# Performance work log

Measured on AMD Instinct MI355X. Metric: run time of the kernel, lower is better.

Reference implementation:

```python
import jax, jax.numpy as jnp
import numpy as np

B, N, K, D, H = 16, 4096, 64, 1024, 8
ITERS = 2
DH = D // H


def _ln(x, g, b, eps=1e-5):
    m = x.mean(-1, keepdims=True)
    v = ((x - m) ** 2).mean(-1, keepdims=True)
    return (x - m) / jnp.sqrt(v + eps) * g + b


def setup_inputs() -> dict:
    key = jax.random.key(0)
    ks = jax.random.split(key, 10)
    def lin(k, fan_in, shape):
        return jax.random.normal(k, shape, jnp.float32) / np.sqrt(fan_in)
    inp = {
        "visual_tokens": jax.random.normal(ks[0], (B, N, D), jnp.float32),
        "slot_init": jax.random.normal(ks[1], (K, D), jnp.float32) * 0.02,
        "ln_vis_g": jnp.ones((D,), jnp.float32), "ln_vis_b": jnp.zeros((D,), jnp.float32),
        "ln_slots_g": jnp.ones((D,), jnp.float32), "ln_slots_b": jnp.zeros((D,), jnp.float32),
        "Wq": lin(ks[2], D, (D, D)),   # [in, out]; y = x @ W
        "Wk": lin(ks[3], D, (D, D)),
        "Wv": lin(ks[4], D, (D, D)),
        "Wo": lin(ks[5], D, (D, D)),
        "mha_in_w": lin(ks[6], D, (3 * D, D)),   # torch layout [3D, D]; y = x @ W.T
        "mha_in_b": jnp.zeros((3 * D,), jnp.float32),
        "mha_out_w": lin(ks[7], D, (D, D)),       # torch layout [D, D]; y = x @ W.T
        "mha_out_b": jnp.zeros((D,), jnp.float32),
        "ln_sa_g": jnp.ones((D,), jnp.float32), "ln_sa_b": jnp.zeros((D,), jnp.float32),
        "ln_ffn_g": jnp.ones((D,), jnp.float32), "ln_ffn_b": jnp.zeros((D,), jnp.float32),
        "W1": lin(ks[8], D, (D, 2 * D)), "b1": jnp.zeros((2 * D,), jnp.float32),
        "W2": lin(ks[9], 2 * D, (2 * D, D)), "b2": jnp.zeros((D,), jnp.float32),
    }
    return inp


def reference(visual_tokens, slot_init, ln_vis_g, ln_vis_b, ln_slots_g, ln_slots_b,
              Wq, Wk, Wv, Wo, mha_in_w, mha_in_b, mha_out_w, mha_out_b,
              ln_sa_g, ln_sa_b, ln_ffn_g, ln_ffn_b, W1, b1, W2, b2):
    scale = D ** -0.5
    vn = _ln(visual_tokens, ln_vis_g, ln_vis_b)          # [B,N,D]
    k = vn @ Wk                                          # constant across iterations
    v = vn @ Wv
    slots = jnp.broadcast_to(slot_init, (B, K, D))
    for _ in range(ITERS):
        sn = _ln(slots, ln_slots_g, ln_slots_b)
        q = sn @ Wq                                      # [B,K,D]
        attn = jnp.einsum('bkd,bnd->bkn', q, k) * scale  # [B,K,N]
        aw = jax.nn.softmax(attn, axis=1)                # softmax over SLOT axis
        slots = slots + jnp.einsum('bkn,bnd->bkd', aw, v) @ Wo
        # slot self-attention (standard MHA, softmax over keys)
        qkv = slots @ mha_in_w.T + mha_in_b              # [B,K,3D]
        mq, mk, mv = jnp.split(qkv, 3, axis=-1)
        def heads(x):
            return x.reshape(B, K, H, DH).transpose(0, 2, 1, 3)  # [B,H,K,DH]
        mq, mk, mv = heads(mq), heads(mk), heads(mv)
        sc = jnp.einsum('bhqd,bhkd->bhqk', mq, mk) / np.sqrt(DH).astype(np.float32)
        p = jax.nn.softmax(sc, axis=-1)
        sa = jnp.einsum('bhqk,bhkd->bhqd', p, mv).transpose(0, 2, 1, 3).reshape(B, K, D)
        sa = sa @ mha_out_w.T + mha_out_b
        slots = _ln(slots + sa, ln_sa_g, ln_sa_b)
    h = _ln(slots, ln_ffn_g, ln_ffn_b)
    return slots + jax.nn.gelu(h @ W1 + b1, approximate=False) @ W2 + b2
```

## Files before the change

### kernel.cpp

```cpp
#include <hip/hip_runtime.h>
#include <math.h>

typedef _Float16 h16;
typedef __attribute__((ext_vector_type(8))) _Float16 half8;
typedef __attribute__((ext_vector_type(4))) float float4v;

#define BB 16
#define NN 4096
#define KK 64
#define DD 1024
#define HH 8

template<int BM, int BN, int WM, int WN, bool SWAP>
__global__ __launch_bounds__(256)
void gemm_nt(const h16* __restrict__ A, const h16* __restrict__ B,
             float* Cf, h16* Ch,
             const float* __restrict__ bias, const float* resid,
             float scale, int Kd, int lda, int ldb, int ldc,
             long sA, long sB, long sC, int act)
{
  constexpr int BK = 32;
  constexpr int WAVES_N = BN / WN;
  constexpr int TM = WM / 16, TN = WN / 16;
  __shared__ alignas(16) h16 Ast[BM * BK];
  __shared__ alignas(16) h16 Bst[BN * BK];
  const int tid  = threadIdx.x;
  const int lane = tid & 63, wave = tid >> 6;
  const int wm = wave / WAVES_N, wn = wave % WAVES_N;
  const int bn = SWAP ? blockIdx.y : blockIdx.x;
  const int bm = SWAP ? blockIdx.x : blockIdx.y;
  const int bz = blockIdx.z;
  const h16* Ab = A + (long)bz * sA;
  const h16* Bb = B + (long)bz * sB;
  const int rowA0 = bm * BM, rowB0 = bn * BN;
  const int lrow = lane >> 2;
  const int lcol = ((lane & 3) ^ (lrow & 3)) * 8;

  float4v acc[TM][TN];
  const float4v fzero = {0.f, 0.f, 0.f, 0.f};
  for (int i = 0; i < TM; i++)
    for (int j = 0; j < TN; j++) acc[i][j] = fzero;

  for (int k0 = 0; k0 < Kd; k0 += BK) {
    __syncthreads();
    for (int c = wave; c < BM/16; c += 4) {
      const h16* g = Ab + (long)(rowA0 + c*16 + lrow) * lda + (k0 + lcol);
      __builtin_amdgcn_global_load_lds((__attribute__((address_space(1))) const void*)g,
          (__attribute__((address_space(3))) void*)(Ast + c*512), 16, 0, 0);
    }
    for (int c = wave; c < BN/16; c += 4) {
      const h16* g = Bb + (long)(rowB0 + c*16 + lrow) * ldb + (k0 + lcol);
      __builtin_amdgcn_global_load_lds((__attribute__((address_space(1))) const void*)g,
          (__attribute__((address_space(3))) void*)(Bst + c*512), 16, 0, 0);
    }
    __syncthreads();

    const int fr = lane & 15;
    const int sw = (((lane >> 4) ^ (fr & 3)) * 8);
    half8 af[TM], bfr[TN];
    #pragma unroll
    for (int t = 0; t < TM; t++)
      af[t] = *(const half8*)(Ast + (wm*WM + t*16 + fr)*BK + sw);
    #pragma unroll
    for (int u = 0; u < TN; u++)
      bfr[u] = *(const half8*)(Bst + (wn*WN + u*16 + fr)*BK + sw);
    #pragma unroll
    for (int t = 0; t < TM; t++)
      #pragma unroll
      for (int u = 0; u < TN; u++)
        acc[t][u] = __builtin_amdgcn_mfma_f32_16x16x32_f16(af[t], bfr[u], acc[t][u], 0, 0, 0);
  }

  const int r0 = rowA0 + wm*WM + (lane >> 4) * 4;
  const int c0 = rowB0 + wn*WN + (lane & 15);
  float* Cfb = Cf ? Cf + (long)bz * sC : (float*)0;
  h16*   Chb = Ch ? Ch + (long)bz * sC : (h16*)0;
  const float* rb = resid ? resid + (long)bz * sC : (const float*)0;
  #pragma unroll
  for (int t = 0; t < TM; t++) {
    #pragma unroll
    for (int u = 0; u < TN; u++) {
      const int col = c0 + u*16;
      const float bv = bias ? bias[col] : 0.f;
      #pragma unroll
      for (int r = 0; r < 4; r++) {
        const long idx = (long)(r0 + t*16 + r) * ldc + col;
        float vv = acc[t][u][r] * scale + bv;
        if (act == 1) vv = 0.5f * vv * (1.f + erff(vv * 0.70710678118654752f));
        if (rb) vv += rb[idx];
        if (Cfb) Cfb[idx] = vv;
        if (Chb) Chb[idx] = (h16)vv;
      }
    }
  }
}

__global__ __launch_bounds__(256)
void attn_softmax(const h16* __restrict__ q, const h16* __restrict__ k,
                  h16* __restrict__ aw)
{
  constexpr int BK = 32;
  __shared__ alignas(16) h16 Ast[64 * BK];
  __shared__ alignas(16) h16 Bst[128 * BK];
  const int tid = threadIdx.x;
  const int lane = tid & 63, wave = tid >> 6;
  const int bn = blockIdx.x, bz = blockIdx.z;
  const h16* Ab = q + (long)bz * (KK * DD);
  const h16* Bb = k + (long)bz * ((long)NN * DD);
  const int rowB0 = bn * 128;
  const int lrow = lane >> 2;
  const int lcol = ((lane & 3) ^ (lrow & 3)) * 8;

  float4v acc[4][2];
  const float4v fzero = {0.f, 0.f, 0.f, 0.f};
  for (int i = 0; i < 4; i++)
    for (int j = 0; j < 2; j++) acc[i][j] = fzero;

  for (int k0 = 0; k0 < DD; k0 += BK) {
    __syncthreads();
    if (wave < 4) {
      const h16* g = Ab + (long)(wave*16 + lrow) * DD + (k0 + lcol);
      __builtin_amdgcn_global_load_lds((__attribute__((address_space(1))) const void*)g,
          (__attribute__((address_space(3))) void*)(Ast + wave*512), 16, 0, 0);
    }
    for (int c = wave; c < 8; c += 4) {
      const h16* g = Bb + (long)(rowB0 + c*16 + lrow) * DD + (k0 + lcol);
      __builtin_amdgcn_global_load_lds((__attribute__((address_space(1))) const void*)g,
          (__attribute__((address_space(3))) void*)(Bst + c*512), 16, 0, 0);
    }
    __syncthreads();
    const int fr = lane & 15;
    const int sw = (((lane >> 4) ^ (fr & 3)) * 8);
    half8 af[4], bfr[2];
    #pragma unroll
    for (int t = 0; t < 4; t++)
      af[t] = *(const half8*)(Ast + (t*16 + fr)*BK + sw);
    #pragma unroll
    for (int u = 0; u < 2; u++)
      bfr[u] = *(const half8*)(Bst + (wave*32 + u*16 + fr)*BK + sw);
    #pragma unroll
    for (int t = 0; t < 4; t++)
      #pragma unroll
      for (int u = 0; u < 2; u++)
        acc[t][u] = __builtin_amdgcn_mfma_f32_16x16x32_f16(af[t], bfr[u], acc[t][u], 0, 0, 0);
  }

  h16* awz = aw + (long)bz * ((long)KK * NN);
  #pragma unroll
  for (int u = 0; u < 2; u++) {
    float e[4][4];
    float mx = -1e30f;
    #pragma unroll
    for (int t = 0; t < 4; t++)
      #pragma unroll
      for (int r = 0; r < 4; r++) {
        e[t][r] = acc[t][u][r] * 0.03125f;
        mx = fmaxf(mx, e[t][r]);
      }
    mx = fmaxf(mx, __shfl_xor(mx, 16));
    mx = fmaxf(mx, __shfl_xor(mx, 32));
    float sum = 0.f;
    #pragma unroll
    for (int t = 0; t < 4; t++)
      #pragma unroll
      for (int r = 0; r < 4; r++) { e[t][r] = __expf(e[t][r] - mx); sum += e[t][r]; }
    sum += __shfl_xor(sum, 16);
    sum += __shfl_xor(sum, 32);
    const float rinv = 1.f / sum;
    const int col = rowB0 + wave*32 + u*16 + (lane & 15);
    #pragma unroll
    for (int t = 0; t < 4; t++)
      #pragma unroll
      for (int r = 0; r < 4; r++) {
        const int row = t*16 + (lane >> 4)*4 + r;
        awz[(long)row * NN + col] = (h16)(e[t][r] * rinv);
      }
  }
}

__global__ __launch_bounds__(256)
void ln_kernel(const float* x, const float* add,
               const float* __restrict__ g, const float* __restrict__ b,
               float* outf, h16* outh)
{
  const int row = blockIdx.x, t = threadIdx.x;
  const long rb_ = (long)row * DD;
  float v[4]; float s = 0.f, s2 = 0.f;
  #pragma unroll
  for (int i = 0; i < 4; i++) {
    const int c = t + i*256;
    float xv = x[rb_ + c];
    if (add) xv += add[rb_ + c];
    v[i] = xv; s += xv; s2 += xv*xv;
  }
  #pragma unroll
  for (int off = 32; off > 0; off >>= 1) {
    s  += __shfl_down(s,  off, 64);
    s2 += __shfl_down(s2, off, 64);
  }
  __shared__ float red[8];
  const int lane = t & 63, w = t >> 6;
  if (lane == 0) { red[w] = s; red[4+w] = s2; }
  __syncthreads();
  const float S  = red[0]+red[1]+red[2]+red[3];
  const float S2 = red[4]+red[5]+red[6]+red[7];
  const float mean = S * (1.f/DD);
  const float var  = S2 * (1.f/DD) - mean*mean;
  const float rinv = rsqrtf(var + 1e-5f);
  #pragma unroll
  for (int i = 0; i < 4; i++) {
    const int c = t + i*256;
    const float y = (v[i] - mean) * rinv * g[c] + b[c];
    if (outf) outf[rb_ + c] = y;
    if (outh) outh[rb_ + c] = (h16)y;
  }
}

__global__ __launch_bounds__(256)
void mha_kernel(const h16* __restrict__ qkv, h16* __restrict__ sa)
{
  const int b = blockIdx.x >> 3, h = blockIdx.x & 7;
  __shared__ h16   mk[64][128];
  __shared__ h16   mv[64][128];
  __shared__ float sc[64][64];
  const int t = threadIdx.x;
  const long base = ((long)b * 64) * (3*DD) + h * 128;
  for (int i = t; i < 64*128; i += 256) {
    const int r = i >> 7, d = i & 127;
    mk[r][d] = qkv[base + (long)r*(3*DD) + DD   + d];
    mv[r][d] = qkv[base + (long)r*(3*DD) + 2*DD + d];
  }
  __syncthreads();
  {
    const int q = t >> 2, kb2 = (t & 3) * 16;
    float accv[16];
    #pragma unroll
    for (int i = 0; i < 16; i++) accv[i] = 0.f;
    const h16* mq = qkv + base + (long)q * (3*DD);
    for (int d0 = 0; d0 < 128; d0 += 8) {
      float qr[8];
      #pragma unroll
      for (int j = 0; j < 8; j++) qr[j] = (float)mq[d0 + j];
      #pragma unroll
      for (int i = 0; i < 16; i++) {
        float sacc = 0.f;
        #pragma unroll
        for (int j = 0; j < 8; j++) sacc += qr[j] * (float)(mk[kb2+i][d0+j]);
        accv[i] += sacc;
      }
    }
    #pragma unroll
    for (int i = 0; i < 16; i++) sc[q][kb2+i] = accv[i] * 0.088388347648318447f;
  }
  __syncthreads();
  if (t < 64) {
    float mx = -1e30f;
    for (int i = 0; i < 64; i++) mx = fmaxf(mx, sc[t][i]);
    float sum = 0.f;
    for (int i = 0; i < 64; i++) { const float e = __expf(sc[t][i] - mx); sc[t][i] = e; sum += e; }
    const float r = 1.f / sum;
    for (int i = 0; i < 64; i++) sc[t][i] *= r;
  }
  __syncthreads();
  {
    const int q = t >> 2, d0 = (t & 3) * 32;
    float o[32];
    #pragma unroll
    for (int i = 0; i < 32; i++) o[i] = 0.f;
    for (int k2 = 0; k2 < 64; k2++) {
      const float p = sc[q][k2];
      #pragma unroll
      for (int i = 0; i < 32; i++) o[i] += p * (float)(mv[k2][d0+i]);
    }
    h16* op = sa + ((long)(b*64 + q)) * DD + h*128 + d0;
    #pragma unroll
    for (int i = 0; i < 32; i++) op[i] = (h16)o[i];
  }
}

__global__ void transpose_cast(const float* __restrict__ src, h16* __restrict__ dst,
                               int R, int C)
{
  __shared__ float tile[32][33];
  const int c0 = blockIdx.x * 32, r0 = blockIdx.y * 32;
  const int tx = threadIdx.x & 31, ty = threadIdx.x >> 5;
  for (int i = ty; i < 32; i += 8) tile[i][tx] = src[(long)(r0+i)*C + c0 + tx];
  __syncthreads();
  for (int i = ty; i < 32; i += 8) dst[(long)(c0+i)*R + r0 + tx] = (h16)tile[tx][i];
}

__global__ void cast_f32_h16(const float* __restrict__ x, h16* __restrict__ y, long n)
{
  const long i = (long)blockIdx.x * 256 + threadIdx.x;
  if (i < n) y[i] = (h16)x[i];
}

__global__ void init_slots(const float* __restrict__ si, float* __restrict__ S)
{
  const long i = (long)blockIdx.x * 256 + threadIdx.x;
  const int row = (int)(i >> 10), d = (int)(i & 1023);
  S[i] = si[((row & 63) << 10) + d];
}

extern "C" void kernel_launch(void* const* d_in, const int* in_sizes, int n_in,
                              void* d_out, int out_size, void* d_ws, size_t ws_size,
                              hipStream_t stream)
{
  const float* vt        = (const float*)d_in[0];
  const float* slot_init = (const float*)d_in[1];
  const float* ln_vis_g  = (const float*)d_in[2];
  const float* ln_vis_b  = (const float*)d_in[3];
  const float* ln_sl_g   = (const float*)d_in[4];
  const float* ln_sl_b   = (const float*)d_in[5];
  const float* Wq        = (const float*)d_in[6];
  const float* Wk        = (const float*)d_in[7];
  const float* Wv        = (const float*)d_in[8];
  const float* Wo        = (const float*)d_in[9];
  const float* mha_in_w  = (const float*)d_in[10];
  const float* mha_in_b  = (const float*)d_in[11];
  const float* mha_out_w = (const float*)d_in[12];
  const float* mha_out_b = (const float*)d_in[13];
  const float* ln_sa_g   = (const float*)d_in[14];
  const float* ln_sa_b   = (const float*)d_in[15];
  const float* ln_ffn_g  = (const float*)d_in[16];
  const float* ln_ffn_b  = (const float*)d_in[17];
  const float* W1        = (const float*)d_in[18];
  const float* b1        = (const float*)d_in[19];
  const float* W2        = (const float*)d_in[20];
  const float* b2        = (const float*)d_in[21];
  float* out = (float*)d_out;

  char* ws = (char*)d_ws;
  size_t off = 0;
  auto alloc = [&](size_t bytes) -> char* {
    char* p = ws + off; off += (bytes + 255) & ~(size_t)255; return p;
  };
  h16* wqT  = (h16*)alloc((size_t)DD*DD*2);
  h16* wkT  = (h16*)alloc((size_t)DD*DD*2);
  h16* wvT  = (h16*)alloc((size_t)DD*DD*2);
  h16* woT  = (h16*)alloc((size_t)DD*DD*2);
  h16* w_in = (h16*)alloc((size_t)3*DD*DD*2);
  h16* w_ou = (h16*)alloc((size_t)DD*DD*2);
  h16* w1T  = (h16*)alloc((size_t)2*DD*DD*2);
  h16* w2T  = (h16*)alloc((size_t)2*DD*DD*2);
  float* S      = (float*)alloc((size_t)BB*KK*DD*4);
  h16*   snb    = (h16*)alloc((size_t)BB*KK*DD*2);
  h16*   qb     = (h16*)alloc((size_t)BB*KK*DD*2);
  h16*   updb   = (h16*)alloc((size_t)BB*KK*DD*2);
  h16*   slotsb = (h16*)alloc((size_t)BB*KK*DD*2);
  h16*   sab    = (h16*)alloc((size_t)BB*KK*DD*2);
  h16*   hb     = (h16*)alloc((size_t)BB*KK*DD*2);
  h16*   g1b    = (h16*)alloc((size_t)BB*KK*2*DD*2);
  h16*   qkvh   = (h16*)alloc((size_t)BB*KK*3*DD*2);
  float* sa2    = (float*)alloc((size_t)BB*KK*DD*4);
  h16*   awb    = (h16*)alloc((size_t)BB*KK*NN*2);
  h16*   vnb    = (h16*)alloc((size_t)BB*NN*DD*2);
  h16*   kbuf   = (h16*)alloc((size_t)BB*NN*DD*2);
  h16*   vT     = (h16*)alloc((size_t)BB*NN*DD*2);
  (void)in_sizes; (void)n_in; (void)out_size; (void)ws_size;

  const dim3 blk(256);
  const float* nf = nullptr;

  transpose_cast<<<dim3(32,32,1), blk, 0, stream>>>(Wq, wqT, DD, DD);
  transpose_cast<<<dim3(32,32,1), blk, 0, stream>>>(Wk, wkT, DD, DD);
  transpose_cast<<<dim3(32,32,1), blk, 0, stream>>>(Wv, wvT, DD, DD);
  transpose_cast<<<dim3(32,32,1), blk, 0, stream>>>(Wo, woT, DD, DD);
  transpose_cast<<<dim3(64,32,1), blk, 0, stream>>>(W1, w1T, DD, 2*DD);
  transpose_cast<<<dim3(32,64,1), blk, 0, stream>>>(W2, w2T, 2*DD, DD);
  cast_f32_h16<<<dim3(12288), blk, 0, stream>>>(mha_in_w, w_in, (long)3*DD*DD);
  cast_f32_h16<<<dim3(4096),  blk, 0, stream>>>(mha_out_w, w_ou, (long)DD*DD);
  init_slots<<<dim3(4096), blk, 0, stream>>>(slot_init, S);

  ln_kernel<<<dim3(BB*NN), blk, 0, stream>>>(vt, nullptr, ln_vis_g, ln_vis_b, nullptr, vnb);
  gemm_nt<128,128,64,64,true><<<dim3(512,8,1), blk, 0, stream>>>(
      vnb, wkT, nullptr, kbuf, nf, nf, 1.f, DD, DD, DD, DD, 0, 0, 0, 0);
  gemm_nt<128,128,64,64,false><<<dim3(32,8,BB), blk, 0, stream>>>(
      wvT, vnb, nullptr, vT, nf, nf, 1.f, DD, DD, DD, NN,
      0, (long)NN*DD, (long)DD*NN, 0);

  for (int it = 0; it < 2; ++it) {
    ln_kernel<<<dim3(BB*KK), blk, 0, stream>>>(S, nullptr, ln_sl_g, ln_sl_b, nullptr, snb);
    gemm_nt<32,64,16,32,false><<<dim3(16,32,1), blk, 0, stream>>>(
        snb, wqT, nullptr, qb, nf, nf, 1.f, DD, DD, DD, DD, 0, 0, 0, 0);
    attn_softmax<<<dim3(32,1,BB), blk, 0, stream>>>(qb, kbuf, awb);
    gemm_nt<32,64,16,32,false><<<dim3(16,2,BB), blk, 0, stream>>>(
        awb, vT, nullptr, updb, nf, nf, 1.f, NN, NN, NN, DD,
        (long)KK*NN, (long)DD*NN, (long)KK*DD, 0);
    gemm_nt<32,64,16,32,false><<<dim3(16,32,1), blk, 0, stream>>>(
        updb, woT, S, slotsb, nf, S, 1.f, DD, DD, DD, DD, 0, 0, 0, 0);
    gemm_nt<64,128,64,32,false><<<dim3(24,16,1), blk, 0, stream>>>(
        slotsb, w_in, nullptr, qkvh, mha_in_b, nf, 1.f, DD, DD, DD, 3*DD, 0, 0, 0, 0);
    mha_kernel<<<dim3(BB*HH), blk, 0, stream>>>(qkvh, sab);
    gemm_nt<32,64,16,32,false><<<dim3(16,32,1), blk, 0, stream>>>(
        sab, w_ou, sa2, nullptr, mha_out_b, nf, 1.f, DD, DD, DD, DD, 0, 0, 0, 0);
    ln_kernel<<<dim3(BB*KK), blk, 0, stream>>>(S, sa2, ln_sa_g, ln_sa_b, S, nullptr);
  }

  ln_kernel<<<dim3(BB*KK), blk, 0, stream>>>(S, nullptr, ln_ffn_g, ln_ffn_b, nullptr, hb);
  gemm_nt<32,128,32,32,false><<<dim3(16,32,1), blk, 0, stream>>>(
      hb, w1T, nullptr, g1b, b1, nf, 1.f, DD, DD, DD, 2*DD, 0, 0, 0, 1);
  gemm_nt<32,64,16,32,false><<<dim3(16,32,1), blk, 0, stream>>>(
      g1b, w2T, out, nullptr, b2, S, 1.f, 2*DD, 2*DD, 2*DD, DD, 0, 0, 0, 0);
}
```

Before: 1.435 ms.

## Add 256x256 8-wave pipelined GEMM with direct-to-LDS loads for K/V projections

Adds a new GEMM kernel with 256x256 output tiles and 512 threads. It loads global memory straight into LDS via global_load_lds into double buffers and interleaves quarter-tile loads with MFMA phases, using barriers and s_setprio. It also remaps blocks across XCDs. The kernel replaces the 128x128 gemm for the large K and V projections, aiming to raise MFMA utilization and cut global traffic per FLOP, at the cost of heavy register and LDS use and intricate synchronization.

```diff
diff --git a/kernel.cpp b/kernel.cpp
--- a/kernel.cpp
+++ b/kernel.cpp
@@ -93,6 +93,214 @@
       }
     }
   }
+}
+
+__device__ __forceinline__ void gld16(const h16* g, h16* l) {
+  __builtin_amdgcn_global_load_lds((__attribute__((address_space(1))) const void*)g,
+                                   (__attribute__((address_space(3))) void*)l, 16, 0, 0);
+}
+
+#define PH_BAR() do { asm volatile("" ::: "memory"); __builtin_amdgcn_s_barrier(); \
+                      asm volatile("" ::: "memory"); } while (0)
+#define WAITV2() asm volatile("s_waitcnt vmcnt(2)" ::: "memory")
+#define WAITV0() asm volatile("s_waitcnt vmcnt(0)" ::: "memory")
+#define MF(a, b, c) c = __builtin_amdgcn_mfma_f32_16x16x32_f16(a, b, c, 0, 0, 0)
+
+template<bool SWAP>
+__global__ __launch_bounds__(512, 2)
+void gemm_nt8(const h16* __restrict__ A, const h16* __restrict__ B,
+              h16* __restrict__ C, int Kd, int lda, int ldb, int ldc,
+              long sA, long sB, long sC, int nInner)
+{
+  __shared__ alignas(16) h16 As[2][16384];
+  __shared__ alignas(16) h16 Bs[2][16384];
+  const int tid  = threadIdx.x;
+  const int lane = tid & 63, wv = tid >> 6;
+  const int wm = wv >> 2, wn = wv & 3;
+  const int fr = lane & 15, fq = lane >> 4;
+
+  const int nwg = gridDim.x;
+  const int q = nwg >> 3, r = nwg & 7;
+  const int xcd = blockIdx.x & 7, lid = blockIdx.x >> 3;
+  const int wg = (xcd < r ? xcd * (q + 1) : r * (q + 1) + (xcd - r) * q) + lid;
+  int bm, bn;
+  if (SWAP) { bm = wg % nInner; bn = wg / nInner; }
+  else      { bn = wg % nInner; bm = wg / nInner; }
+  const int bz = blockIdx.z;
+
+  const h16* pA = A + (long)bz * sA + (long)(bm * 256) * lda;
+  const h16* pB = B + (long)bz * sB + (long)(bn * 256) * ldb;
+
+  const int srow = tid >> 3;
+  const int scol = ((tid & 7) ^ (srow & 7)) << 3;
+  const h16* stA = pA + (long)srow * lda + scol;
+  const h16* stB = pB + (long)srow * ldb + scol;
+  const int nt = Kd >> 6;
+
+  auto stage = [&](int t, int hf) {
+    if (t >= nt) return;
+    const int d = t & 1;
+    if (hf < 2) {
+      const h16* g = stA + (long)(hf * 128) * lda + t * 64;
+      h16* l = &As[d][hf * 8192] + wv * 512;
+      gld16(g, l);
+      gld16(g + (long)64 * lda, l + 4096);
+    } else {
+      const h16* g = stB + (long)((hf - 2) * 128) * ldb + t * 64;
+      h16* l = &Bs[d][(hf - 2) * 8192] + wv * 512;
+      gld16(g, l);
+      gld16(g + (long)64 * ldb, l + 4096);
+    }
+  };
+
+  const int rbA = (wm * 128 + fr) * 64;
+  const int rbB = (wn * 64 + fr) * 64;
+  const int cs0 = ((fq)     ^ (fr & 7)) << 3;
+  const int cs1 = ((4 + fq) ^ (fr & 7)) << 3;
+
+  float4v acc[8][4];
+  const float4v fzero = {0.f, 0.f, 0.f, 0.f};
+  #pragma unroll
+  for (int m = 0; m < 8; m++)
+    #pragma unroll
+    for (int n = 0; n < 4; n++) acc[m][n] = fzero;
+
+  stage(0, 0); stage(0, 1); stage(0, 2); stage(0, 3);
+  stage(1, 0);
+  if (nt > 1) WAITV2(); else WAITV0();
+  __builtin_amdgcn_s_barrier();
+  asm volatile("" ::: "memory");
+
+  half8 aL[4][2], aH[4][2], bL[2][2], bH[2][2];
+
+  for (int T = 0; T < nt; T += 2) {
+    #pragma unroll
+    for (int m = 0; m < 4; m++) {
+      aL[m][0] = *(const half8*)&As[0][rbA + m*1024 + cs0];
+      aL[m][1] = *(const half8*)&As[0][rbA + m*1024 + cs1];
+    }
+    #pragma unroll
+    for (int n = 0; n < 2; n++) {
+      bL[n][0] = *(const half8*)&Bs[0][rbB + n*1024 + cs0];
+      bL[n][1] = *(const half8*)&Bs[0][rbB + n*1024 + cs1];
+    }
+    stage(T + 1, 1);
+    PH_BAR();
+    __builtin_amdgcn_s_setprio(1);
+    #pragma unroll
+    for (int m = 0; m < 4; m++)
+      #pragma unroll
+      for (int n = 0; n < 2; n++) { MF(aL[m][0], bL[n][0], acc[m][n]); MF(aL[m][1], bL[n][1], acc[m][n]); }
+    __builtin_amdgcn_s_setprio(0);
+    PH_BAR();
+    #pragma unroll
+    for (int n = 0; n < 2; n++) {
+      bH[n][0] = *(const half8*)&Bs[0][rbB + (n+2)*1024 + cs0];
+      bH[n][1] = *(const half8*)&Bs[0][rbB + (n+2)*1024 + cs1];
+    }
+    stage(T + 1, 2);
+    PH_BAR();
+    __builtin_amdgcn_s_setprio(1);
+    #pragma unroll
+    for (int m = 0; m < 4; m++)
+      #pragma unroll
+      for (int n = 0; n < 2; n++) { MF(aL[m][0], bH[n][0], acc[m][n+2]); MF(aL[m][1], bH[n][1], acc[m][n+2]); }
+    __builtin_amdgcn_s_setprio(0);
+    PH_BAR();
+    #pragma unroll
+    for (int m = 0; m < 4; m++) {
+      aH[m][0] = *(const half8*)&As[0][rbA + (m+4)*1024 + cs0];
+      aH[m][1] = *(const half8*)&As[0][rbA + (m+4)*1024 + cs1];
+    }
+    stage(T + 1, 3);
+    PH_BAR();
+    __builtin_amdgcn_s_setprio(1);
+    #pragma unroll
+    for (int m = 0; m < 4; m++)
+      #pragma unroll
+      for (int n = 0; n < 2; n++) { MF(aH[m][0], bH[n][0], acc[m+4][n+2]); MF(aH[m][1], bH[n][1], acc[m+4][n+2]); }
+    __builtin_amdgcn_s_setprio(0);
+    PH_BAR();
+    stage(T + 2, 0);
+    PH_BAR();
+    __builtin_amdgcn_s_setprio(1);
+    #pragma unroll
+    for (int m = 0; m < 4; m++)
+      #pragma unroll
+      for (int n = 0; n < 2; n++) { MF(aH[m][0], bL[n][0], acc[m+4][n]); MF(aH[m][1], bL[n][1], acc[m+4][n]); }
+    __builtin_amdgcn_s_setprio(0);
+    if (T + 2 < nt) WAITV2(); else WAITV0();
+    PH_BAR();
+
+    #pragma unroll
+    for (int m = 0; m < 4; m++) {
+      aL[m][0] = *(const half8*)&As[1][rbA + m*1024 + cs0];
+      aL[m][1] = *(const half8*)&As[1][rbA + m*1024 + cs1];
+    }
+    #pragma unroll
+    for (int n = 0; n < 2; n++) {
+      bL[n][0] = *(const half8*)&Bs[1][rbB + n*1024 + cs0];
+      bL[n][1] = *(const half8*)&Bs[1][rbB + n*1024 + cs1];
+    }
+    stage(T + 2, 1);
+    PH_BAR();
+    __builtin_amdgcn_s_setprio(1);
+    #pragma unroll
+    for (int m = 0; m < 4; m++)
+      #pragma unroll
+      for (int n = 0; n < 2; n++) { MF(aL[m][0], bL[n][0], acc[m][n]); MF(aL[m][1], bL[n][1], acc[m][n]); }
+    __builtin_amdgcn_s_setprio(0);
+    PH_BAR();
+    #pragma unroll
+    for (int n = 0; n < 2; n++) {
+      bH[n][0] = *(const half8*)&Bs[1][rbB + (n+2)*1024 + cs0];
+      bH[n][1] = *(const half8*)&Bs[1][rbB + (n+2)*1024 + cs1];
+    }
+    stage(T + 2, 2);
+    PH_BAR();
+    __builtin_amdgcn_s_setprio(1);
+    #pragma unroll
+    for (int m = 0; m < 4; m++)
+      #pragma unroll
+      for (int n = 0; n < 2; n++) { MF(aL[m][0], bH[n][0], acc[m][n+2]); MF(aL[m][1], bH[n][1], acc[m][n+2]); }
+    __builtin_amdgcn_s_setprio(0);
+    PH_BAR();
+    #pragma unroll
+    for (int m = 0; m < 4; m++) {
+      aH[m][0] = *(const half8*)&As[1][rbA + (m+4)*1024 + cs0];
+      aH[m][1] = *(const half8*)&As[1][rbA + (m+4)*1024 + cs1];
+    }
+    stage(T + 2, 3);
+    PH_BAR();
+    __builtin_amdgcn_s_setprio(1);
+    #pragma unroll
+    for (int m = 0; m < 4; m++)
+      #pragma unroll
+      for (int n = 0; n < 2; n++) { MF(aH[m][0], bH[n][0], acc[m+4][n+2]); MF(aH[m][1], bH[n][1], acc[m+4][n+2]); }
+    __builtin_amdgcn_s_setprio(0);
+    PH_BAR();
+    stage(T + 3, 0);
+    PH_BAR();
+    __builtin_amdgcn_s_setprio(1);
+    #pragma unroll
+    for (int m = 0; m < 4; m++)
+      #pragma unroll
+      for (int n = 0; n < 2; n++) { MF(aH[m][0], bL[n][0], acc[m+4][n]); MF(aH[m][1], bL[n][1], acc[m+4][n]); }
+    __builtin_amdgcn_s_setprio(0);
+    if (T + 3 < nt) WAITV2(); else WAITV0();
+    PH_BAR();
+  }
+
+  h16* Cb = C + (long)bz * sC;
+  const int r0 = bm * 256 + wm * 128 + fq * 4;
+  const int c0 = bn * 256 + wn * 64 + fr;
+  #pragma unroll
+  for (int m = 0; m < 8; m++)
+    #pragma unroll
+    for (int n = 0; n < 4; n++)
+      #pragma unroll
+      for (int rr = 0; rr < 4; rr++)
+        Cb[(long)(r0 + m*16 + rr) * ldc + (c0 + n*16)] = (h16)acc[m][n][rr];
 }
 
 __global__ __launch_bounds__(256)
@@ -360,6 +568,7 @@
   (void)in_sizes; (void)n_in; (void)out_size; (void)ws_size;
 
   const dim3 blk(256);
+  const dim3 blk8(512);
   const float* nf = nullptr;
 
   transpose_cast<<<dim3(32,32,1), blk, 0, stream>>>(Wq, wqT, DD, DD);
@@ -373,11 +582,10 @@
   init_slots<<<dim3(4096), blk, 0, stream>>>(slot_init, S);
 
   ln_kernel<<<dim3(BB*NN), blk, 0, stream>>>(vt, nullptr, ln_vis_g, ln_vis_b, nullptr, vnb);
-  gemm_nt<128,128,64,64,true><<<dim3(512,8,1), blk, 0, stream>>>(
-      vnb, wkT, nullptr, kbuf, nf, nf, 1.f, DD, DD, DD, DD, 0, 0, 0, 0);
-  gemm_nt<128,128,64,64,false><<<dim3(32,8,BB), blk, 0, stream>>>(
-      wvT, vnb, nullptr, vT, nf, nf, 1.f, DD, DD, DD, NN,
-      0, (long)NN*DD, (long)DD*NN, 0);
+  gemm_nt8<false><<<dim3(1024,1,1), blk8, 0, stream>>>(
+      vnb, wkT, kbuf, DD, DD, DD, DD, 0, 0, 0, 4);
+  gemm_nt8<true><<<dim3(64,1,BB), blk8, 0, stream>>>(
+      wvT, vnb, vT, DD, DD, DD, NN, 0, (long)NN*DD, (long)DD*NN, 4);
 
   for (int it = 0; it < 2; ++it) {
     ln_kernel<<<dim3(BB*KK), blk, 0, stream>>>(S, nullptr, ln_sl_g, ln_sl_b, nullptr, snb);
```

New measurement: 1.303 ms. 1.1x faster.
